# Optimization experiments

Measured on AMD Instinct MI355X. Metric: run time of the kernel, lower is better.

## Reference

```python
import jax, jax.numpy as jnp
import numpy as np

B, C_IN, H, W = 16, 16, 64, 64
C_OUT, KH, KW, DH, DW = 16, 3, 3, 1, 1
OH = (H - KH) // DH + 1  # 62
OW = (W - KW) // DW + 1  # 62


def setup_inputs() -> dict:
    key = jax.random.key(0)
    k1, k2 = jax.random.split(key)
    x = jax.random.normal(k1, (B, C_IN, H, W), dtype=jnp.float32)
    weight = jax.random.normal(k2, (1, C_OUT, C_IN, OH, OW, KH * KW), dtype=jnp.float32)
    return {"x": x, "weight": weight}


def _extract_patches(x):
    # Equivalent to torch unfold(2,kh,dh).unfold(3,kw,dw).view(..., kh*kw):
    # patches[b,c,y,x,k] with k = i*KW + j (row-major over kernel window).
    slabs = [x[:, :, i:i + OH * DH:DH, j:j + OW * DW:DW]
             for i in range(KH) for j in range(KW)]
    return jnp.stack(slabs, axis=-1)  # [B, C_IN, OH, OW, KH*KW]


def reference(x, weight):
    patches = _extract_patches(x)
    # out[b,o,y,x] = sum_{c,k} patches[b,c,y,x,k] * weight[0,o,c,y,x,k]
    out = jnp.einsum('bcyxk,ocyxk->boyx', patches, weight[0])
    return out
```

## Files before the change

### kernel.cpp

```cpp
#include <hip/hip_runtime.h>


#define CIN   16
#define COUT  16
#define HH    64
#define WW    64
#define OHH   62
#define OWW   62
#define HW    (HH * WW)

#define WOSTR (CIN * OHH * OWW * 9)
#define WCSTR (OHH * OWW * 9)
#define NC    8
#define OTILE 288

__global__ __launch_bounds__(256)
void zero_out(float* __restrict__ outg) {
    ((float4*)outg)[blockIdx.x * 256 + threadIdx.x] = make_float4(0.f, 0.f, 0.f, 0.f);
}

__global__ __launch_bounds__(256, 2)
void lc2d(const float* __restrict__ xg,
          const float* __restrict__ wg,
          float* __restrict__ outg)
{
    __shared__ float Wl[2][8 * OTILE];

    const int tid = threadIdx.x;
    const int y   = blockIdx.x;
    const int xh  = blockIdx.y;
    const int oh  = blockIdx.z & 1;
    const int ch  = blockIdx.z >> 1;
    const int x0  = xh * 32;
    const int cstart = ch * NC;

    const int xl  = tid & 31;
    const int og  = (tid >> 5) & 1;
    const int bg  = tid >> 6;
    const int pos = x0 + xl;
    const bool valid = pos < OWW;
    const int xp  = valid ? pos : (OWW - 1);

    const int q   = tid >> 5;
    const int sxi = tid & 31;
    const int sx  = (x0 + sxi < OWW) ? (x0 + sxi) : (OWW - 1);
    const float* wst = wg + (size_t)(oh * 8 + q) * WOSTR + (size_t)cstart * WCSTR
                          + (size_t)(y * OWW + sx) * 9;
    const int wrbase = q * OTILE + sxi;

    {
        float pf[9];
        #pragma unroll
        for (int r = 0; r < 9; ++r) pf[r] = wst[r];
        #pragma unroll
        for (int r = 0; r < 9; ++r) Wl[0][wrbase + r * 32] = pf[r];
    }
    __syncthreads();

    float acc[4][4];
    #pragma unroll
    for (int t = 0; t < 4; ++t)
        #pragma unroll
        for (int b = 0; b < 4; ++b) acc[t][b] = 0.f;

    const float* xbb = xg + ((size_t)(bg * 4) * CIN + cstart) * HW
                          + (size_t)y * WW + xp;

    for (int cc = 0; cc < NC; ++cc) {
        const float* cur = Wl[cc & 1];
        float*       nxt = Wl[(cc + 1) & 1];

        float xv[4][9];
        #pragma unroll
        for (int b = 0; b < 4; ++b) {
            const float* xr = xbb + ((size_t)b * CIN + cc) * HW;
            #pragma unroll
            for (int i = 0; i < 3; ++i)
                #pragma unroll
                for (int j = 0; j < 3; ++j)
                    xv[b][i * 3 + j] = xr[i * WW + j];
        }

        float pf[9];
        if (cc + 1 < NC) {
            const float* ws = wst + (size_t)(cc + 1) * WCSTR;
            #pragma unroll
            for (int r = 0; r < 9; ++r) pf[r] = ws[r];
        }

        #pragma unroll
        for (int t = 0; t < 4; ++t) {
            const float* wb = &cur[(og * 4 + t) * OTILE + xl];
            float wv[9];
            #pragma unroll
            for (int k = 0; k < 9; ++k) wv[k] = wb[k * 32];
            #pragma unroll
            for (int b = 0; b < 4; ++b) {
                float s = acc[t][b];
                #pragma unroll
                for (int k = 0; k < 9; ++k)
                    s = fmaf(wv[k], xv[b][k], s);
                acc[t][b] = s;
            }
        }

        if (cc + 1 < NC) {
            #pragma unroll
            for (int r = 0; r < 9; ++r) nxt[wrbase + r * 32] = pf[r];
            __syncthreads();
        }
    }

    if (valid) {
        #pragma unroll
        for (int t = 0; t < 4; ++t) {
            const int o = oh * 8 + og * 4 + t;
            #pragma unroll
            for (int b = 0; b < 4; ++b) {
                const int bb = bg * 4 + b;
                atomicAdd(&outg[((size_t)(bb * COUT + o) * OHH + y) * OWW + pos],
                          acc[t][b]);
            }
        }
    }
}

extern "C" void kernel_launch(void* const* d_in, const int* in_sizes, int n_in,
                              void* d_out, int out_size, void* d_ws, size_t ws_size,
                              hipStream_t stream) {
    const float* x = (const float*)d_in[0];
    const float* w = (const float*)d_in[1];
    float* out = (float*)d_out;

    zero_out<<<dim3(961), dim3(256), 0, stream>>>(out);
    dim3 grid(OHH, 2, 4);
    lc2d<<<grid, dim3(256), 0, stream>>>(x, w, out);
}
```

Measured before the change: 94.32 us.

## Drop LDS weight staging and channel split, use register double-buffered vector loads

Removes the shared-memory weight tile and its barriers. Each thread now loads its 9-tap weights and input rows directly from global memory as float4 vectors, double-buffered in registers across all 16 input channels. Because one block now covers every input channel, the output is written with plain stores, so the atomics and the separate zero-fill kernel go away. In exchange, several threads reload the same weights and rely on the caches to absorb the repeats. The float4 loads also read slightly past the valid window, and at the very last position this may step just beyond the end of the buffer.

```diff
diff --git a/kernel.cpp b/kernel.cpp
--- a/kernel.cpp
+++ b/kernel.cpp
@@ -11,103 +11,102 @@
 
 #define WOSTR (CIN * OHH * OWW * 9)
 #define WCSTR (OHH * OWW * 9)
-#define NC    8
-#define OTILE 288
-
-__global__ __launch_bounds__(256)
-void zero_out(float* __restrict__ outg) {
-    ((float4*)outg)[blockIdx.x * 256 + threadIdx.x] = make_float4(0.f, 0.f, 0.f, 0.f);
-}
 
 __global__ __launch_bounds__(256, 2)
 void lc2d(const float* __restrict__ xg,
           const float* __restrict__ wg,
           float* __restrict__ outg)
 {
-    __shared__ float Wl[2][8 * OTILE];
-
     const int tid = threadIdx.x;
     const int y   = blockIdx.x;
-    const int xh  = blockIdx.y;
-    const int oh  = blockIdx.z & 1;
-    const int ch  = blockIdx.z >> 1;
-    const int x0  = xh * 32;
-    const int cstart = ch * NC;
+    const int xq  = blockIdx.y;
+    const int oh  = blockIdx.z;
+    const int x0  = xq * 16;
 
-    const int xl  = tid & 31;
-    const int og  = (tid >> 5) & 1;
-    const int bg  = tid >> 6;
+    const int xl  = tid & 15;
+    const int us  = (tid >> 4) & 3;
+    const int v   = tid >> 6;
+    const int og  = v >> 1;
+    const int bb  = ((v & 1) * 4 + us) * 2;
+
     const int pos = x0 + xl;
     const bool valid = pos < OWW;
     const int xp  = valid ? pos : (OWW - 1);
 
-    const int q   = tid >> 5;
-    const int sxi = tid & 31;
-    const int sx  = (x0 + sxi < OWW) ? (x0 + sxi) : (OWW - 1);
-    const float* wst = wg + (size_t)(oh * 8 + q) * WOSTR + (size_t)cstart * WCSTR
-                          + (size_t)(y * OWW + sx) * 9;
-    const int wrbase = q * OTILE + sxi;
+    const float* wbase = wg + (size_t)(oh * 8 + og * 4) * WOSTR
+                            + (size_t)(y * OWW + xp) * 9;
+    const float* xbase = xg + (size_t)bb * CIN * HW + (size_t)y * WW + xp;
 
-    {
-        float pf[9];
+    float wv[2][4][9];
+    float xv[2][2][12];
+
+    #pragma unroll
+    for (int t = 0; t < 4; ++t) {
+        const float* p = wbase + (size_t)t * WOSTR;
+        float4 A = *(const float4*)p;
+        float4 Bv = *(const float4*)(p + 4);
+        float  c8 = p[8];
+        wv[0][t][0] = A.x;  wv[0][t][1] = A.y;  wv[0][t][2] = A.z;  wv[0][t][3] = A.w;
+        wv[0][t][4] = Bv.x; wv[0][t][5] = Bv.y; wv[0][t][6] = Bv.z; wv[0][t][7] = Bv.w;
+        wv[0][t][8] = c8;
+    }
+    #pragma unroll
+    for (int bi = 0; bi < 2; ++bi) {
+        const float* p = xbase + (size_t)bi * CIN * HW;
         #pragma unroll
-        for (int r = 0; r < 9; ++r) pf[r] = wst[r];
-        #pragma unroll
-        for (int r = 0; r < 9; ++r) Wl[0][wrbase + r * 32] = pf[r];
+        for (int i = 0; i < 3; ++i) {
+            float4 r = *(const float4*)(p + i * WW);
+            xv[0][bi][i * 4 + 0] = r.x;
+            xv[0][bi][i * 4 + 1] = r.y;
+            xv[0][bi][i * 4 + 2] = r.z;
+        }
     }
-    __syncthreads();
 
-    float acc[4][4];
+    float acc[4][2];
     #pragma unroll
-    for (int t = 0; t < 4; ++t)
-        #pragma unroll
-        for (int b = 0; b < 4; ++b) acc[t][b] = 0.f;
+    for (int t = 0; t < 4; ++t) { acc[t][0] = 0.f; acc[t][1] = 0.f; }
 
-    const float* xbb = xg + ((size_t)(bg * 4) * CIN + cstart) * HW
-                          + (size_t)y * WW + xp;
+    #pragma unroll
+    for (int c = 0; c < CIN; ++c) {
+        const int cu = c & 1;
+        const int nu = cu ^ 1;
 
-    for (int cc = 0; cc < NC; ++cc) {
-        const float* cur = Wl[cc & 1];
-        float*       nxt = Wl[(cc + 1) & 1];
-
-        float xv[4][9];
-        #pragma unroll
-        for (int b = 0; b < 4; ++b) {
-            const float* xr = xbb + ((size_t)b * CIN + cc) * HW;
+        if (c + 1 < CIN) {
             #pragma unroll
-            for (int i = 0; i < 3; ++i)
+            for (int bi = 0; bi < 2; ++bi) {
+                const float* p = xbase + (size_t)bi * CIN * HW + (size_t)(c + 1) * HW;
                 #pragma unroll
-                for (int j = 0; j < 3; ++j)
-                    xv[b][i * 3 + j] = xr[i * WW + j];
-        }
-
-        float pf[9];
-        if (cc + 1 < NC) {
-            const float* ws = wst + (size_t)(cc + 1) * WCSTR;
+                for (int i = 0; i < 3; ++i) {
+                    float4 r = *(const float4*)(p + i * WW);
+                    xv[nu][bi][i * 4 + 0] = r.x;
+                    xv[nu][bi][i * 4 + 1] = r.y;
+                    xv[nu][bi][i * 4 + 2] = r.z;
+                }
+            }
             #pragma unroll
-            for (int r = 0; r < 9; ++r) pf[r] = ws[r];
+            for (int t = 0; t < 4; ++t) {
+                const float* p = wbase + (size_t)t * WOSTR + (size_t)(c + 1) * WCSTR;
+                float4 A = *(const float4*)p;
+                float4 Bv = *(const float4*)(p + 4);
+                float  c8 = p[8];
+                wv[nu][t][0] = A.x;  wv[nu][t][1] = A.y;  wv[nu][t][2] = A.z;  wv[nu][t][3] = A.w;
+                wv[nu][t][4] = Bv.x; wv[nu][t][5] = Bv.y; wv[nu][t][6] = Bv.z; wv[nu][t][7] = Bv.w;
+                wv[nu][t][8] = c8;
+            }
         }
 
         #pragma unroll
         for (int t = 0; t < 4; ++t) {
-            const float* wb = &cur[(og * 4 + t) * OTILE + xl];
-            float wv[9];
             #pragma unroll
-            for (int k = 0; k < 9; ++k) wv[k] = wb[k * 32];
-            #pragma unroll
-            for (int b = 0; b < 4; ++b) {
-                float s = acc[t][b];
+            for (int bi = 0; bi < 2; ++bi) {
+                float s = acc[t][bi];
                 #pragma unroll
-                for (int k = 0; k < 9; ++k)
-                    s = fmaf(wv[k], xv[b][k], s);
-                acc[t][b] = s;
+                for (int k = 0; k < 9; ++k) {
+                    const int xi = (k / 3) * 4 + (k % 3);
+                    s = fmaf(wv[cu][t][k], xv[cu][bi][xi], s);
+                }
+                acc[t][bi] = s;
             }
-        }
-
-        if (cc + 1 < NC) {
-            #pragma unroll
-            for (int r = 0; r < 9; ++r) nxt[wrbase + r * 32] = pf[r];
-            __syncthreads();
         }
     }
 
@@ -116,10 +115,9 @@
         for (int t = 0; t < 4; ++t) {
             const int o = oh * 8 + og * 4 + t;
             #pragma unroll
-            for (int b = 0; b < 4; ++b) {
-                const int bb = bg * 4 + b;
-                atomicAdd(&outg[((size_t)(bb * COUT + o) * OHH + y) * OWW + pos],
-                          acc[t][b]);
+            for (int bi = 0; bi < 2; ++bi) {
+                const int b = bb + bi;
+                outg[((size_t)(b * COUT + o) * OHH + y) * OWW + pos] = acc[t][bi];
             }
         }
     }
@@ -132,7 +130,6 @@
     const float* w = (const float*)d_in[1];
     float* out = (float*)d_out;
 
-    zero_out<<<dim3(961), dim3(256), 0, stream>>>(out);
-    dim3 grid(OHH, 2, 4);
+    dim3 grid(OHH, 4, 2);
     lc2d<<<grid, dim3(256), 0, stream>>>(x, w, out);
 }
```

Measured after the change: 160.2 us. 69.8% more time.
